# Performance work log

Hardware: AMD Instinct MI355X
Metric: run time of the kernel (lower is better)

The kernel has to match this reference:

```python
import jax, jax.numpy as jnp
import numpy as np

N_ACT = 3  # [relu, tanh, sigmoid]


def setup_inputs() -> dict:
    key = jax.random.key(0)
    k1, k2, k3 = jax.random.split(key, 3)
    B, IN, OUT = 4096, 4096, 4096
    x = jax.random.normal(k1, (B, IN), dtype=jnp.float32)
    W = jax.random.normal(k2, (OUT, IN), dtype=jnp.float32)
    b = jax.random.normal(k3, (OUT,), dtype=jnp.float32)
    return {"x": x, "W": W, "b": b}


def reference(x, W, b):
    # Linear: y = x @ W^T + b  -> [B, OUT]
    y = jnp.einsum("bi,oi->bo", x, W) + b
    # Per-output-column criterion: mean over batch, then idx = int(mean % 3).
    # torch `%` on tensors is remainder with the divisor's sign (non-negative
    # here), and int() then truncates == floor for non-negative values.
    means = jnp.mean(y, axis=0)                        # [OUT]
    idx = jnp.mod(means, float(N_ACT)).astype(jnp.int32)  # [OUT] in {0,1,2}
    idx_b = idx[None, :]                               # broadcast over batch
    # Device-side branchless select among the three activations.
    out = jnp.where(
        idx_b == 0,
        jax.nn.relu(y),
        jnp.where(idx_b == 1, jnp.tanh(y), jax.nn.sigmoid(y)),
    )
    return out
```

## Files before the change

### kernel.cpp

```cpp
#include <hip/hip_runtime.h>
#include <hip/hip_bf16.h>
#include <math.h>

#define B_DIM   4096
#define IN_DIM  4096
#define OUT_DIM 4096

typedef __attribute__((ext_vector_type(8))) short  short8;
typedef __attribute__((ext_vector_type(4))) float  floatx4;

__device__ __forceinline__ ushort f2bf(float f) {
    unsigned b = __float_as_uint(f);
    return (ushort)((b + 0x7fffu + ((b >> 16) & 1u)) >> 16);
}

__global__ void cvt_x_colsum(const float* __restrict__ x, ushort* __restrict__ xb,
                             double* __restrict__ part) {
    int c0 = blockIdx.x * 1024 + threadIdx.x * 4;
    int r0 = blockIdx.y * 16;
    double s0 = 0, s1 = 0, s2 = 0, s3 = 0;
#pragma unroll 4
    for (int r = 0; r < 16; ++r) {
        size_t off = (size_t)(r0 + r) * IN_DIM + c0;
        float4 v = *(const float4*)(x + off);
        ushort4 o;
        o.x = f2bf(v.x); o.y = f2bf(v.y); o.z = f2bf(v.z); o.w = f2bf(v.w);
        *(ushort4*)(xb + off) = o;
        s0 += (double)v.x; s1 += (double)v.y; s2 += (double)v.z; s3 += (double)v.w;
    }
    double* p = part + (size_t)blockIdx.y * IN_DIM + c0;
    p[0] = s0; p[1] = s1; p[2] = s2; p[3] = s3;
}

__global__ void xbar_reduce(const double* __restrict__ part, double* __restrict__ xbar) {
    int i = blockIdx.x * 256 + threadIdx.x;
    double s = 0.0;
    for (int rb = 0; rb < 256; ++rb) s += part[(size_t)rb * IN_DIM + i];
    xbar[i] = s * (1.0 / (double)B_DIM);
}

__global__ void cvt_w_means(const float* __restrict__ W, const float* __restrict__ bias,
                            const double* __restrict__ xbar, ushort* __restrict__ wb,
                            int* __restrict__ idx) {
    __shared__ double red[256];
    int o = blockIdx.x;
    size_t base = (size_t)o * IN_DIM;
    double s = 0.0;
#pragma unroll
    for (int j = 0; j < 4; ++j) {
        int i = j * 1024 + threadIdx.x * 4;
        float4 v = *(const float4*)(W + base + i);
        ushort4 ob;
        ob.x = f2bf(v.x); ob.y = f2bf(v.y); ob.z = f2bf(v.z); ob.w = f2bf(v.w);
        *(ushort4*)(wb + base + i) = ob;
        s += (double)v.x * xbar[i]     + (double)v.y * xbar[i + 1]
           + (double)v.z * xbar[i + 2] + (double)v.w * xbar[i + 3];
    }
    red[threadIdx.x] = s;
    __syncthreads();
    for (int st = 128; st > 0; st >>= 1) {
        if (threadIdx.x < st) red[threadIdx.x] += red[threadIdx.x + st];
        __syncthreads();
    }
    if (threadIdx.x == 0) {
        float mf = (float)(red[0] + (double)bias[o]);
        float md = fmodf(mf, 3.0f);
        if (md < 0.0f) md += 3.0f;
        idx[o] = (int)md;
    }
}

__global__ void __launch_bounds__(256) gemm_bt_act(
    const ushort* __restrict__ A,
    const ushort* __restrict__ Bt,
    const float*  __restrict__ bias,
    const int*    __restrict__ idx,
    float*        __restrict__ out) {
    __shared__ __align__(16) ushort As[128 * 32];
    __shared__ __align__(16) ushort Bs[128 * 32];

    const int t    = threadIdx.x;
    const int w    = t >> 6;
    const int l    = t & 63;
    const int quad = l >> 4;
    const int lrow = l & 15;
    const int m0   = blockIdx.y * 128;
    const int n0   = blockIdx.x * 128;
    const int m0w  = (w >> 1) * 64;
    const int n0w  = (w & 1) * 64;
    const int K    = IN_DIM;

    floatx4 acc[4][4] = {};

    for (int k0 = 0; k0 < K; k0 += 32) {
#pragma unroll
        for (int j = 0; j < 2; ++j) {
            int chunk  = j * 256 + t;
            int r      = chunk >> 2;
            int kc     = (chunk & 3) << 3;
            int ldsoff = (j * 256 + w * 64) * 8;
            __builtin_amdgcn_global_load_lds(
                (__attribute__((address_space(1))) void*)(A + (size_t)(m0 + r) * K + k0 + kc),
                (__attribute__((address_space(3))) void*)(As + ldsoff), 16, 0, 0);
            __builtin_amdgcn_global_load_lds(
                (__attribute__((address_space(1))) void*)(Bt + (size_t)(n0 + r) * K + k0 + kc),
                (__attribute__((address_space(3))) void*)(Bs + ldsoff), 16, 0, 0);
        }
        __syncthreads();

        short8 af[4], bf[4];
#pragma unroll
        for (int mi = 0; mi < 4; ++mi)
            af[mi] = *(const short8*)&As[(m0w + mi * 16 + lrow) * 32 + quad * 8];
#pragma unroll
        for (int ni = 0; ni < 4; ++ni)
            bf[ni] = *(const short8*)&Bs[(n0w + ni * 16 + lrow) * 32 + quad * 8];

#pragma unroll
        for (int mi = 0; mi < 4; ++mi)
#pragma unroll
            for (int ni = 0; ni < 4; ++ni)
                acc[mi][ni] = __builtin_amdgcn_mfma_f32_16x16x32_bf16(
                    af[mi], bf[ni], acc[mi][ni], 0, 0, 0);
        __syncthreads();
    }

#pragma unroll
    for (int ni = 0; ni < 4; ++ni) {
        int   col     = n0 + n0w + ni * 16 + lrow;
        int   id      = idx[col];
        float bv      = bias[col];
        float a       = (id == 1) ? -2.0f : -1.0f;
        bool  isrelu  = (id == 0);
        bool  istanh  = (id == 1);
#pragma unroll
        for (int mi = 0; mi < 4; ++mi) {
            int rowb = m0 + m0w + mi * 16 + quad * 4;
#pragma unroll
            for (int r = 0; r < 4; ++r) {
                float y   = acc[mi][ni][r] + bv;
                float e   = __expf(a * y);
                float s   = __builtin_amdgcn_rcpf(1.0f + e);
                float act = istanh ? fmaf(2.0f, s, -1.0f) : s;
                float v   = isrelu ? fmaxf(y, 0.0f) : act;
                out[(size_t)(rowb + r) * OUT_DIM + col] = v;
            }
        }
    }
}

extern "C" void kernel_launch(void* const* d_in, const int* in_sizes, int n_in,
                              void* d_out, int out_size, void* d_ws, size_t ws_size,
                              hipStream_t stream) {
    const float* x = (const float*)d_in[0];
    const float* W = (const float*)d_in[1];
    const float* b = (const float*)d_in[2];
    float* out = (float*)d_out;

    char* ws = (char*)d_ws;
    ushort* xb   = (ushort*)(ws);
    ushort* wb   = (ushort*)(ws + (33554432));
    double* part = (double*)(ws + (67108864));
    double* xbar = (double*)(ws + (67108864 + 8388608));
    int*    idx  = (int*)   (ws + (67108864 + 8388608 + 32768));

    cvt_x_colsum<<<dim3(4, 256), 256, 0, stream>>>(x, xb, part);
    xbar_reduce<<<16, 256, 0, stream>>>(part, xbar);
    cvt_w_means<<<4096, 256, 0, stream>>>(W, b, xbar, wb, idx);
    gemm_bt_act<<<dim3(32, 32), 256, 0, stream>>>(xb, wb, b, idx, out);
}
```

Before: 365.8 us.

## Double GEMM K-tile with XOR-swizzled LDS, grouped block order, parallel xbar reduce

The GEMM now stages 64-wide K tiles instead of 32, which halves the number of barrier pairs per K sweep. It applies an XOR swizzle on 16-byte chunks in LDS to avoid bank conflicts on the MFMA fragment reads. Blocks are remapped into 8x8 supertiles so neighbouring workgroups share A and B rows in L2. The xbar reduction is split across four row slices per column with an LDS combine so it uses more blocks, and cvt_w_means loads xbar as double2 vectors. The larger LDS footprint may lower occupancy, and there is still no software pipelining across tiles.

```diff
diff --git a/kernel.cpp b/kernel.cpp
--- a/kernel.cpp
+++ b/kernel.cpp
@@ -33,10 +33,19 @@
 }
 
 __global__ void xbar_reduce(const double* __restrict__ part, double* __restrict__ xbar) {
-    int i = blockIdx.x * 256 + threadIdx.x;
+    __shared__ double red[256];
+    int col   = blockIdx.x * 64 + (threadIdx.x & 63);
+    int slice = threadIdx.x >> 6;
     double s = 0.0;
-    for (int rb = 0; rb < 256; ++rb) s += part[(size_t)rb * IN_DIM + i];
-    xbar[i] = s * (1.0 / (double)B_DIM);
+    for (int rb = slice * 64; rb < slice * 64 + 64; ++rb)
+        s += part[(size_t)rb * IN_DIM + col];
+    red[threadIdx.x] = s;
+    __syncthreads();
+    if (slice == 0) {
+        double v = red[threadIdx.x] + red[threadIdx.x + 64]
+                 + red[threadIdx.x + 128] + red[threadIdx.x + 192];
+        xbar[col] = v * (1.0 / (double)B_DIM);
+    }
 }
 
 __global__ void cvt_w_means(const float* __restrict__ W, const float* __restrict__ bias,
@@ -53,8 +62,10 @@
         ushort4 ob;
         ob.x = f2bf(v.x); ob.y = f2bf(v.y); ob.z = f2bf(v.z); ob.w = f2bf(v.w);
         *(ushort4*)(wb + base + i) = ob;
-        s += (double)v.x * xbar[i]     + (double)v.y * xbar[i + 1]
-           + (double)v.z * xbar[i + 2] + (double)v.w * xbar[i + 3];
+        double2 xv0 = *(const double2*)(xbar + i);
+        double2 xv1 = *(const double2*)(xbar + i + 2);
+        s += (double)v.x * xv0.x + (double)v.y * xv0.y
+           + (double)v.z * xv1.x + (double)v.w * xv1.y;
     }
     red[threadIdx.x] = s;
     __syncthreads();
@@ -76,52 +87,66 @@
     const float*  __restrict__ bias,
     const int*    __restrict__ idx,
     float*        __restrict__ out) {
-    __shared__ __align__(16) ushort As[128 * 32];
-    __shared__ __align__(16) ushort Bs[128 * 32];
+    __shared__ __align__(16) ushort As[128 * 64];
+    __shared__ __align__(16) ushort Bs[128 * 64];
 
     const int t    = threadIdx.x;
     const int w    = t >> 6;
     const int l    = t & 63;
     const int quad = l >> 4;
     const int lrow = l & 15;
-    const int m0   = blockIdx.y * 128;
-    const int n0   = blockIdx.x * 128;
+
+    const int b   = blockIdx.y * 32 + blockIdx.x;
+    const int sup = b >> 6;
+    const int q   = b & 63;
+    const int m0  = ((sup >> 2) * 8 + (q >> 3)) * 128;
+    const int n0  = ((sup & 3)  * 8 + (q & 7))  * 128;
+
     const int m0w  = (w >> 1) * 64;
     const int n0w  = (w & 1) * 64;
     const int K    = IN_DIM;
 
     floatx4 acc[4][4] = {};
 
-    for (int k0 = 0; k0 < K; k0 += 32) {
+    for (int k0 = 0; k0 < K; k0 += 64) {
 #pragma unroll
-        for (int j = 0; j < 2; ++j) {
-            int chunk  = j * 256 + t;
-            int r      = chunk >> 2;
-            int kc     = (chunk & 3) << 3;
+        for (int j = 0; j < 4; ++j) {
+            int chunk = j * 256 + t;
+            int r     = chunk >> 3;
+            int kb    = (chunk & 7) ^ (r & 7);
+            int goff  = kb << 3;
             int ldsoff = (j * 256 + w * 64) * 8;
             __builtin_amdgcn_global_load_lds(
-                (__attribute__((address_space(1))) void*)(A + (size_t)(m0 + r) * K + k0 + kc),
+                (__attribute__((address_space(1))) void*)(A + (size_t)(m0 + r) * K + k0 + goff),
                 (__attribute__((address_space(3))) void*)(As + ldsoff), 16, 0, 0);
             __builtin_amdgcn_global_load_lds(
-                (__attribute__((address_space(1))) void*)(Bt + (size_t)(n0 + r) * K + k0 + kc),
+                (__attribute__((address_space(1))) void*)(Bt + (size_t)(n0 + r) * K + k0 + goff),
                 (__attribute__((address_space(3))) void*)(Bs + ldsoff), 16, 0, 0);
         }
         __syncthreads();
 
-        short8 af[4], bf[4];
 #pragma unroll
-        for (int mi = 0; mi < 4; ++mi)
-            af[mi] = *(const short8*)&As[(m0w + mi * 16 + lrow) * 32 + quad * 8];
+        for (int s = 0; s < 2; ++s) {
+            short8 af[4], bf[4];
 #pragma unroll
-        for (int ni = 0; ni < 4; ++ni)
-            bf[ni] = *(const short8*)&Bs[(n0w + ni * 16 + lrow) * 32 + quad * 8];
-
+            for (int mi = 0; mi < 4; ++mi) {
+                int r = m0w + mi * 16 + lrow;
+                int kb = (s * 4 + quad) ^ (r & 7);
+                af[mi] = *(const short8*)&As[r * 64 + kb * 8];
+            }
 #pragma unroll
-        for (int mi = 0; mi < 4; ++mi)
+            for (int ni = 0; ni < 4; ++ni) {
+                int r = n0w + ni * 16 + lrow;
+                int kb = (s * 4 + quad) ^ (r & 7);
+                bf[ni] = *(const short8*)&Bs[r * 64 + kb * 8];
+            }
 #pragma unroll
-            for (int ni = 0; ni < 4; ++ni)
-                acc[mi][ni] = __builtin_amdgcn_mfma_f32_16x16x32_bf16(
-                    af[mi], bf[ni], acc[mi][ni], 0, 0, 0);
+            for (int mi = 0; mi < 4; ++mi)
+#pragma unroll
+                for (int ni = 0; ni < 4; ++ni)
+                    acc[mi][ni] = __builtin_amdgcn_mfma_f32_16x16x32_bf16(
+                        af[mi], bf[ni], acc[mi][ni], 0, 0, 0);
+        }
         __syncthreads();
     }
 
@@ -165,7 +190,7 @@
     int*    idx  = (int*)   (ws + (67108864 + 8388608 + 32768));
 
     cvt_x_colsum<<<dim3(4, 256), 256, 0, stream>>>(x, xb, part);
-    xbar_reduce<<<16, 256, 0, stream>>>(part, xbar);
+    xbar_reduce<<<64, 256, 0, stream>>>(part, xbar);
     cvt_w_means<<<4096, 256, 0, stream>>>(W, b, xbar, wb, idx);
     gemm_bt_act<<<dim3(32, 32), 256, 0, stream>>>(xb, wb, b, idx, out);
 }
```

Result: faster. 344.4 us (-5.8%).
